# Kernel tuning notes

Hardware: AMD Instinct MI355X
Metric: run time of the kernel (lower is better)

The kernel has to match this reference:

```python
import jax, jax.numpy as jnp
import numpy as np

B, L, D, H, Dh = 4, 2048, 1024, 16, 64
DECAY_LR, A_LR, V_LR, G_LR = 64, 64, 32, 128
EPS_GN = 0.00064


def _lora(x, A, Bm, b, act):
    h = x @ A.T
    if act is not None:
        h = act(h)
    y = h @ Bm.T
    return y if b is None else y + b


def setup_inputs() -> dict:
    key = jax.random.key(0)
    ks = jax.random.split(key, 32)
    n = lambda k, shape, s=0.02: (jax.random.normal(k, shape, jnp.float32) * s)
    return {
        "x": n(ks[0], (B, L, D), 1.0),
        "v_first": n(ks[1], (B, L, H, Dh), 1.0),
        "x_r": n(ks[2], (1, 1, D)), "x_w": n(ks[3], (1, 1, D)),
        "x_k": n(ks[4], (1, 1, D)), "x_v": n(ks[5], (1, 1, D)),
        "x_a": n(ks[6], (1, 1, D)), "x_g": n(ks[7], (1, 1, D)),
        "k_k": n(ks[8], (H, Dh), 0.5), "k_a": n(ks[9], (H, Dh), 0.5),
        "r_k": n(ks[10], (H, Dh), 0.5),
        "Wr": n(ks[11], (D, D)), "Wk": n(ks[12], (D, D)),
        "Wv": n(ks[13], (D, D)), "Wo": n(ks[14], (D, D)),
        "gn_w": 1.0 + n(ks[15], (H, Dh)), "gn_b": n(ks[16], (H, Dh)),
        "w_A": n(ks[17], (DECAY_LR, D)), "w_B": n(ks[18], (D, DECAY_LR)), "w_b": n(ks[19], (D,)),
        "v_A": n(ks[20], (V_LR, D)), "v_B": n(ks[21], (D, V_LR)), "v_b": n(ks[22], (D,)),
        "a_A": n(ks[23], (A_LR, D)), "a_B": n(ks[24], (D, A_LR)), "a_b": n(ks[25], (D,)),
        "g_A": n(ks[26], (G_LR, D)), "g_B": n(ks[27], (D, G_LR)),
    }


def reference(x, v_first, x_r, x_w, x_k, x_v, x_a, x_g, k_k, k_a, r_k,
              Wr, Wk, Wv, Wo, gn_w, gn_b,
              w_A, w_B, w_b, v_A, v_B, v_b, a_A, a_B, a_b, g_A, g_B):
    Bx, Lx, Dx = x.shape
    # token shift (no cache -> zero-padded shift)
    x_prev = jnp.concatenate([jnp.zeros_like(x[:, :1]), x[:, :-1]], axis=1)
    xx = x_prev - x
    xr = x + xx * x_r
    xw = x + xx * x_w
    xk = x + xx * x_k
    xv = x + xx * x_v
    xa = x + xx * x_a
    xg = x + xx * x_g

    r = (xr @ Wr.T).reshape(Bx, Lx, H, Dh)
    k = (xk @ Wk.T).reshape(Bx, Lx, H, Dh)
    v = (xv @ Wv.T).reshape(Bx, Lx, H, Dh)
    iclr = jax.nn.sigmoid(_lora(xa, a_A, a_B, a_b, None)).reshape(Bx, Lx, H, Dh)
    gate = _lora(xg, g_A, g_B, None, jax.nn.sigmoid)  # (B,L,D)

    # layer_idx > 0: residual value mixing with v_first
    vv = jax.nn.sigmoid(_lora(xv, v_A, v_B, v_b, None)).reshape(Bx, Lx, H, Dh)
    v = v + (v_first - v) * vv

    w = jnp.exp(-0.606531 * jax.nn.sigmoid(
        _lora(xw, w_A, w_B, w_b, jnp.tanh)).reshape(Bx, Lx, H, Dh))

    kkn = k * k_k
    kk = kkn / jnp.maximum(jnp.linalg.norm(kkn, axis=-1, keepdims=True), 1e-7)
    k = k * (1.0 + (iclr - 1.0) * k_a)
    a = -kk
    b = kk * iclr

    # WKV7 generalized delta-rule scan over time
    def step(state, inp):
        rt, wt, kt, vt, at, bt = inp  # each (B,H,Dh)
        sa = jnp.einsum('bhij,bhj->bhi', state, at)
        state = (state * wt[:, :, None, :]
                 + vt[..., :, None] * kt[..., None, :]
                 + sa[..., :, None] * bt[..., None, :])
        y = jnp.einsum('bhij,bhj->bhi', state, rt)
        return state, y

    tr = lambda z: jnp.swapaxes(z, 0, 1)  # (B,L,H,Dh) -> (L,B,H,Dh)
    state0 = jnp.zeros((Bx, H, Dh, Dh), x.dtype)
    _, ys = jax.lax.scan(step, state0, (tr(r), tr(w), tr(k), tr(v), tr(a), tr(b)))
    out = jnp.swapaxes(ys, 0, 1)  # (B,L,H,Dh)

    # per-head layernorm (group norm), eps = 0.00064
    mean = out.mean(axis=-1, keepdims=True)
    var = out.var(axis=-1, keepdims=True)
    out = gn_w * (out - mean) / jnp.sqrt(var + EPS_GN) + gn_b

    out = out + jnp.sum(r * k * r_k, axis=-1, keepdims=True) * v
    out = out.reshape(Bx, Lx, Dx)
    return (out * gate) @ Wo.T
```

## Files before the change

kernel.cpp:

```cpp
#include <hip/hip_runtime.h>
#include <cmath>


#define DEV __device__ __forceinline__

typedef unsigned short u16;
typedef unsigned int u32;
typedef __bf16 bf16x8 __attribute__((ext_vector_type(8)));
typedef float f32x4 __attribute__((ext_vector_type(4)));

constexpr int Bx = 4, Lx = 2048, Dx = 1024, Hx = 16, Dh = 64;
constexpr int NTOK = Bx * Lx;
constexpr float EPS_GN = 0.00064f;
constexpr int STEP_U16 = 384;
constexpr int TB = 16;
constexpr int NB = Lx / TB;
constexpr int BATCH_U16 = TB * STEP_U16;

DEV float bf2f(u16 u) { union { u32 i; float f; } c; c.i = ((u32)u) << 16; return c.f; }
DEV u16 f2bf(float f) {
    union { float f; u32 i; } c; c.f = f;
    u32 r = c.i + 0x7FFFu + ((c.i >> 16) & 1u);
    return (u16)(r >> 16);
}
DEV void unpack2(u32 u, float& a, float& b) {
    union { u32 i; float f; } c0, c1;
    c0.i = u << 16; c1.i = u & 0xFFFF0000u;
    a = c0.f; b = c1.f;
}

template <int CTRL>
DEV float dpp_add(float v) {
    int p = __builtin_amdgcn_update_dpp(0, __float_as_int(v), CTRL, 0xF, 0xF, true);
    return v + __int_as_float(p);
}

DEV float xor32_add(float x) {
    float a = x, b = x;
    asm volatile("s_nop 1\n\tv_permlane32_swap_b32 %0, %1" : "+v"(a), "+v"(b));
    return a + b;
}

DEV float red32(float x) {
    x = dpp_add<0xB1>(x);
    x = dpp_add<0x4E>(x);
    x = dpp_add<0x141>(x);
    x = dpp_add<0x140>(x);
    return xor32_add(x);
}

__global__ __launch_bounds__(256) void conv_kernel(
    const float* s0, const float* s1, const float* s2, const float* s3,
    const float* s4, const float* s5, const float* s6, const float* s7,
    const float* s8, const float* s9, const float* s10, const float* s11,
    u16* d0, u16* d1, u16* d2, u16* d3, u16* d4, u16* d5, u16* d6, u16* d7,
    u16* d8, u16* d9, u16* d10, u16* d11)
{
    const float* srcs[12] = {s0,s1,s2,s3,s4,s5,s6,s7,s8,s9,s10,s11};
    u16* dsts[12] = {d0,d1,d2,d3,d4,d5,d6,d7,d8,d9,d10,d11};
    const int ns[12] = {65536,65536,32768,32768,65536,65536,131072,131072,
                        1048576,1048576,1048576,1048576};
    int t = blockIdx.y;
    int i = (blockIdx.x * 256 + threadIdx.x) * 4;
    if (i >= ns[t]) return;
    float4 v = *(const float4*)(srcs[t] + i);
    ushort4 o;
    o.x = f2bf(v.x); o.y = f2bf(v.y); o.z = f2bf(v.z); o.w = f2bf(v.w);
    *(ushort4*)(dsts[t] + i) = o;
}

__global__ __launch_bounds__(256) void mix_kernel(
    const float* __restrict__ x,
    const float* __restrict__ mr, const float* __restrict__ mw, const float* __restrict__ mk,
    const float* __restrict__ mv, const float* __restrict__ ma, const float* __restrict__ mg,
    u16* __restrict__ XR, u16* __restrict__ XW, u16* __restrict__ XK,
    u16* __restrict__ XV, u16* __restrict__ XA, u16* __restrict__ XG)
{
    int gi = blockIdx.x * 256 + threadIdx.x;
    int n  = gi >> 8;
    int d4 = (gi & 255) << 2;
    int l  = n & (Lx - 1);
    size_t o = (size_t)n * Dx + d4;
    float4 xc = *(const float4*)(x + o);
    float4 xp = make_float4(0.f, 0.f, 0.f, 0.f);
    if (l != 0) xp = *(const float4*)(x + o - Dx);
    float dx0 = xp.x - xc.x, dx1 = xp.y - xc.y, dx2 = xp.z - xc.z, dx3 = xp.w - xc.w;
    const float* mvs[6] = {mr, mw, mk, mv, ma, mg};
    u16* dsts[6] = {XR, XW, XK, XV, XA, XG};
#pragma unroll
    for (int j = 0; j < 6; ++j) {
        float4 m = *(const float4*)(mvs[j] + d4);
        ushort4 r;
        r.x = f2bf(fmaf(dx0, m.x, xc.x));
        r.y = f2bf(fmaf(dx1, m.y, xc.y));
        r.z = f2bf(fmaf(dx2, m.z, xc.z));
        r.w = f2bf(fmaf(dx3, m.w, xc.w));
        *(ushort4*)(dsts[j] + o) = r;
    }
}

template <int BN, int ACT, bool BIAS, bool F32OUT>
DEV void gemm_body(const u16* __restrict__ A, const u16* __restrict__ B16,
                   const float* __restrict__ bias, void* __restrict__ Cv,
                   int M, int N, int K, int bx, int by)
{
    constexpr int BM = 128, BK = 32;
    constexpr int WGM = (BN == 128) ? 2 : 4;
    constexpr int WGN = (BN == 128) ? 2 : 1;
    constexpr int WTM = BM / WGM, WTN = BN / WGN;
    constexpr int ITM = WTM / 16, ITN = WTN / 16;
    __shared__ __align__(16) u16 Asm[BM * BK];
    __shared__ __align__(16) u16 Bsm[BN * BK];
    const int tid = threadIdx.x;
    const int wid = tid >> 6, lane = tid & 63;
    const int q = lane >> 4, r16 = lane & 15;
    const size_t m0 = (size_t)bx * BM;
    const size_t n0 = (size_t)by * BN;
    const int wm = (wid % WGM) * WTM;
    const int wn = (wid / WGM) * WTN;
    f32x4 acc[ITM][ITN];
    const f32x4 zf = {0.f, 0.f, 0.f, 0.f};
#pragma unroll
    for (int i = 0; i < ITM; ++i)
#pragma unroll
        for (int j = 0; j < ITN; ++j) acc[i][j] = zf;

    for (int k0 = 0; k0 < K; k0 += BK) {
#pragma unroll
        for (int it = 0; it < 2; ++it) {
            int base = it * 2048 + wid * 512;
            int pp = base + lane * 8;
            int row = pp >> 5, col = pp & 31;
            __builtin_amdgcn_global_load_lds(
                (const __attribute__((address_space(1))) void*)(A + (m0 + row) * K + k0 + col),
                (__attribute__((address_space(3))) void*)(Asm + base), 16, 0, 0);
        }
#pragma unroll
        for (int it = 0; it < (BN * BK + 2047) / 2048; ++it) {
            int base = it * 2048 + wid * 512;
            if (BN * BK >= 2048 || base < BN * BK) {
                int pp = base + lane * 8;
                int row = pp >> 5, col = pp & 31;
                __builtin_amdgcn_global_load_lds(
                    (const __attribute__((address_space(1))) void*)(B16 + (n0 + row) * K + k0 + col),
                    (__attribute__((address_space(3))) void*)(Bsm + base), 16, 0, 0);
            }
        }
        __syncthreads();
        bf16x8 af[ITM], bfr[ITN];
#pragma unroll
        for (int im = 0; im < ITM; ++im)
            af[im] = *(const bf16x8*)&Asm[(wm + im * 16 + r16) * BK + q * 8];
#pragma unroll
        for (int in = 0; in < ITN; ++in)
            bfr[in] = *(const bf16x8*)&Bsm[(wn + in * 16 + r16) * BK + q * 8];
#pragma unroll
        for (int im = 0; im < ITM; ++im)
#pragma unroll
            for (int in = 0; in < ITN; ++in)
                acc[im][in] = __builtin_amdgcn_mfma_f32_16x16x32_bf16(af[im], bfr[in], acc[im][in], 0, 0, 0);
        __syncthreads();
    }
#pragma unroll
    for (int im = 0; im < ITM; ++im) {
#pragma unroll
        for (int in = 0; in < ITN; ++in) {
#pragma unroll
            for (int e = 0; e < 4; ++e) {
                size_t row = m0 + wm + im * 16 + q * 4 + e;
                size_t col = n0 + wn + in * 16 + r16;
                float val = acc[im][in][e];
                if constexpr (BIAS) val += bias[col];
                if constexpr (ACT == 1) val = 1.f / (1.f + __expf(-val));
                else if constexpr (ACT == 2) val = tanhf(val);
                else if constexpr (ACT == 3) val = __expf(-0.606531f / (1.f + __expf(-val)));
                if constexpr (F32OUT) ((float*)Cv)[row * (size_t)N + col] = val;
                else ((u16*)Cv)[row * (size_t)N + col] = f2bf(val);
            }
        }
    }
}

DEV void gemm_body_rt(const u16* __restrict__ A, const u16* __restrict__ B16,
                      const float* __restrict__ bias, u16* __restrict__ C,
                      int N, int K, int act, int bx, int by)
{
    constexpr int BM = 128, BN = 128, BK = 32;
    constexpr int ITM = 4, ITN = 4;
    __shared__ __align__(16) u16 Asm[BM * BK];
    __shared__ __align__(16) u16 Bsm[BN * BK];
    const int tid = threadIdx.x;
    const int wid = tid >> 6, lane = tid & 63;
    const int q = lane >> 4, r16 = lane & 15;
    const size_t m0 = (size_t)bx * BM;
    const size_t n0 = (size_t)by * BN;
    const int wm = (wid % 2) * 64;
    const int wn = (wid / 2) * 64;
    f32x4 acc[ITM][ITN];
    const f32x4 zf = {0.f, 0.f, 0.f, 0.f};
#pragma unroll
    for (int i = 0; i < ITM; ++i)
#pragma unroll
        for (int j = 0; j < ITN; ++j) acc[i][j] = zf;

    for (int k0 = 0; k0 < K; k0 += BK) {
#pragma unroll
        for (int it = 0; it < 2; ++it) {
            int base = it * 2048 + wid * 512;
            int pp = base + lane * 8;
            int row = pp >> 5, col = pp & 31;
            __builtin_amdgcn_global_load_lds(
                (const __attribute__((address_space(1))) void*)(A + (m0 + row) * K + k0 + col),
                (__attribute__((address_space(3))) void*)(Asm + base), 16, 0, 0);
        }
#pragma unroll
        for (int it = 0; it < 2; ++it) {
            int base = it * 2048 + wid * 512;
            int pp = base + lane * 8;
            int row = pp >> 5, col = pp & 31;
            __builtin_amdgcn_global_load_lds(
                (const __attribute__((address_space(1))) void*)(B16 + (n0 + row) * K + k0 + col),
                (__attribute__((address_space(3))) void*)(Bsm + base), 16, 0, 0);
        }
        __syncthreads();
        bf16x8 af[ITM], bfr[ITN];
#pragma unroll
        for (int im = 0; im < ITM; ++im)
            af[im] = *(const bf16x8*)&Asm[(wm + im * 16 + r16) * BK + q * 8];
#pragma unroll
        for (int in = 0; in < ITN; ++in)
            bfr[in] = *(const bf16x8*)&Bsm[(wn + in * 16 + r16) * BK + q * 8];
#pragma unroll
        for (int im = 0; im < ITM; ++im)
#pragma unroll
            for (int in = 0; in < ITN; ++in)
                acc[im][in] = __builtin_amdgcn_mfma_f32_16x16x32_bf16(af[im], bfr[in], acc[im][in], 0, 0, 0);
        __syncthreads();
    }
#pragma unroll
    for (int im = 0; im < ITM; ++im) {
#pragma unroll
        for (int in = 0; in < ITN; ++in) {
#pragma unroll
            for (int e = 0; e < 4; ++e) {
                size_t row = m0 + wm + im * 16 + q * 4 + e;
                size_t col = n0 + wn + in * 16 + r16;
                float val = acc[im][in][e];
                if (bias) val += bias[col];
                if (act == 1) val = 1.f / (1.f + __expf(-val));
                else if (act == 3) val = __expf(-0.606531f / (1.f + __expf(-val)));
                C[row * (size_t)N + col] = f2bf(val);
            }
        }
    }
}

DEV void lora1_body(int cfg,
    const u16* __restrict__ XW, const u16* __restrict__ XA,
    const u16* __restrict__ XV, const u16* __restrict__ XG,
    const u16* __restrict__ wAB, const u16* __restrict__ aAB,
    const u16* __restrict__ vAB, const u16* __restrict__ gAB,
    u16* __restrict__ HW, u16* __restrict__ HA,
    u16* __restrict__ HV, u16* __restrict__ HG, int bx)
{
    constexpr int BM = 128, BK = 32, K = 1024;
    constexpr int ITM = 2, ITN = 4;
    const u16* A; const u16* Bm; u16* C; int ldC, Nv, act;
    if (cfg == 0)      { A = XW; Bm = wAB;            C = HW;      ldC = 64;  Nv = 64; act = 2; }
    else if (cfg == 1) { A = XA; Bm = aAB;            C = HA;      ldC = 64;  Nv = 64; act = 0; }
    else if (cfg == 2) { A = XV; Bm = vAB;            C = HV;      ldC = 32;  Nv = 32; act = 0; }
    else if (cfg == 3) { A = XG; Bm = gAB;            C = HG;      ldC = 128; Nv = 64; act = 1; }
    else               { A = XG; Bm = gAB + 64 * K;   C = HG + 64; ldC = 128; Nv = 64; act = 1; }

    __shared__ __align__(16) u16 Asm1[BM * BK];
    __shared__ __align__(16) u16 Bsm1[64 * BK];
    const int tid = threadIdx.x;
    const int wid = tid >> 6, lane = tid & 63;
    const int q = lane >> 4, r16 = lane & 15;
    const size_t m0 = (size_t)bx * BM;
    const int wm = wid * 32;
    f32x4 acc[ITM][ITN];
    const f32x4 zf = {0.f, 0.f, 0.f, 0.f};
#pragma unroll
    for (int i = 0; i < ITM; ++i)
#pragma unroll
        for (int j = 0; j < ITN; ++j) acc[i][j] = zf;

    for (int k0 = 0; k0 < K; k0 += BK) {
#pragma unroll
        for (int it = 0; it < 2; ++it) {
            int base = it * 2048 + wid * 512;
            int pp = base + lane * 8;
            int row = pp >> 5, col = pp & 31;
            __builtin_amdgcn_global_load_lds(
                (const __attribute__((address_space(1))) void*)(A + (m0 + row) * K + k0 + col),
                (__attribute__((address_space(3))) void*)(Asm1 + base), 16, 0, 0);
        }
        {
            int base = wid * 512;
            int pp = base + lane * 8;
            int row = pp >> 5, col = pp & 31;
            __builtin_amdgcn_global_load_lds(
                (const __attribute__((address_space(1))) void*)(Bm + row * K + k0 + col),
                (__attribute__((address_space(3))) void*)(Bsm1 + base), 16, 0, 0);
        }
        __syncthreads();
        bf16x8 af[ITM], bfr[ITN];
#pragma unroll
        for (int im = 0; im < ITM; ++im)
            af[im] = *(const bf16x8*)&Asm1[(wm + im * 16 + r16) * BK + q * 8];
#pragma unroll
        for (int in = 0; in < ITN; ++in)
            bfr[in] = *(const bf16x8*)&Bsm1[(in * 16 + r16) * BK + q * 8];
#pragma unroll
        for (int im = 0; im < ITM; ++im)
#pragma unroll
            for (int in = 0; in < ITN; ++in)
                acc[im][in] = __builtin_amdgcn_mfma_f32_16x16x32_bf16(af[im], bfr[in], acc[im][in], 0, 0, 0);
        __syncthreads();
    }
#pragma unroll
    for (int im = 0; im < ITM; ++im) {
#pragma unroll
        for (int in = 0; in < ITN; ++in) {
#pragma unroll
            for (int e = 0; e < 4; ++e) {
                size_t row = m0 + wm + im * 16 + q * 4 + e;
                int col = in * 16 + r16;
                if (col < Nv) {
                    float val = acc[im][in][e];
                    if (act == 1) val = 1.f / (1.f + __expf(-val));
                    else if (act == 2) val = tanhf(val);
                    C[row * (size_t)ldC + col] = f2bf(val);
                }
            }
        }
    }
}

__global__ __launch_bounds__(256) void proj_kernel(
    const u16* __restrict__ XR, const u16* __restrict__ XK, const u16* __restrict__ XV,
    const u16* __restrict__ XW, const u16* __restrict__ XA, const u16* __restrict__ XG,
    const u16* __restrict__ Wr16, const u16* __restrict__ Wk16, const u16* __restrict__ Wv16,
    const u16* __restrict__ wAB, const u16* __restrict__ aAB,
    const u16* __restrict__ vAB, const u16* __restrict__ gAB,
    u16* __restrict__ Rbuf, u16* __restrict__ Kbuf, u16* __restrict__ Vbuf,
    u16* __restrict__ HW, u16* __restrict__ HA, u16* __restrict__ HV, u16* __restrict__ HG)
{
    const int z = blockIdx.z;
    if (z < 3) {
        const u16* A; const u16* Bm; u16* C;
        if (z == 0)      { A = XR; Bm = Wr16; C = Rbuf; }
        else if (z == 1) { A = XK; Bm = Wk16; C = Kbuf; }
        else             { A = XV; Bm = Wv16; C = Vbuf; }
        gemm_body<128, 0, false, false>(A, Bm, nullptr, C, NTOK, 1024, 1024,
                                        blockIdx.x, blockIdx.y);
    } else {
        if (blockIdx.y >= 5) return;
        lora1_body(blockIdx.y, XW, XA, XV, XG, wAB, aAB, vAB, gAB, HW, HA, HV, HG,
                   blockIdx.x);
    }
}

__global__ __launch_bounds__(256) void lora2_kernel(
    const u16* __restrict__ HW, const u16* __restrict__ HA,
    const u16* __restrict__ HV, const u16* __restrict__ HG,
    const u16* __restrict__ wBB, const u16* __restrict__ aBB,
    const u16* __restrict__ vBB, const u16* __restrict__ gBB,
    const float* __restrict__ wb, const float* __restrict__ ab, const float* __restrict__ vb,
    u16* __restrict__ Wdec16, u16* __restrict__ ICLR,
    u16* __restrict__ VVb, u16* __restrict__ GATE)
{
    const int z = blockIdx.z;
    const u16* A; const u16* Bm; const float* bias; u16* C; int K, act;
    if (z == 0)      { A = HW; Bm = wBB; bias = wb;      C = Wdec16; K = 64;  act = 3; }
    else if (z == 1) { A = HA; Bm = aBB; bias = ab;      C = ICLR;   K = 64;  act = 1; }
    else if (z == 2) { A = HV; Bm = vBB; bias = vb;      C = VVb;    K = 32;  act = 1; }
    else             { A = HG; Bm = gBB; bias = nullptr; C = GATE;   K = 128; act = 0; }
    gemm_body_rt(A, Bm, bias, C, 1024, K, act, blockIdx.x, blockIdx.y);
}

__global__ __launch_bounds__(256) void gemm_out_kernel(
    const u16* __restrict__ A, const u16* __restrict__ B16, float* __restrict__ C)
{
    gemm_body<128, 0, false, true>(A, B16, nullptr, C, NTOK, 1024, 1024,
                                   blockIdx.x, blockIdx.y);
}

__global__ __launch_bounds__(256) void prep_pack_kernel(
    const u16* __restrict__ Kb, const u16* __restrict__ Vb,
    const u16* __restrict__ Rb, const u16* __restrict__ Wd16,
    const u16* __restrict__ ICLR, const u16* __restrict__ VVb, const float* __restrict__ vfirst,
    const float* __restrict__ k_k, const float* __restrict__ k_a,
    u16* __restrict__ stream)
{
    int g = blockIdx.x * 4 + (threadIdx.x >> 6);
    int lane = threadIdx.x & 63;
    int h = g & (Hx - 1);
    int n = g >> 4;
    size_t idx = (size_t)g * 64 + lane;
    int hd = h * 64 + lane;
    int l = n & (Lx - 1), b = n >> 11;
    size_t so = ((size_t)((b * 16 + h) * Lx + l)) * STEP_U16;

    float k = bf2f(Kb[idx]);
    float iclr = bf2f(ICLR[idx]);
    float kkn = k * k_k[hd];
    float s = kkn * kkn;
#pragma unroll
    for (int off = 32; off > 0; off >>= 1) s += __shfl_xor(s, off, 64);
    float nrm = fmaxf(sqrtf(s), 1e-7f);
    float kk = kkn / nrm;
    u16 knew = f2bf(k * (1.f + (iclr - 1.f) * k_a[hd]));
    float v = bf2f(Vb[idx]), vv = bf2f(VVb[idx]), vf = vfirst[idx];
    u16 vnew = f2bf(fmaf(vf - v, vv, v));
    stream[so + lane]       = Rb[idx];
    stream[so + 64 + lane]  = knew;
    stream[so + 128 + lane] = f2bf(-kk);
    stream[so + 192 + lane] = f2bf(kk * iclr);
    stream[so + 256 + lane] = vnew;
    stream[so + 320 + lane] = Wd16[idx];
}

__global__ __launch_bounds__(256, 2) void scan_kernel(
    const u16* __restrict__ stream, float* __restrict__ Y)
{
    const int bid = blockIdx.x;
    const int xcd = bid & 7, slot = bid >> 3;
    const int bh = xcd + ((slot & 7) << 3);
    const int part = slot >> 3;
    const int tid = threadIdx.x;
    const int lane = tid & 63;
    const int w = tid >> 6;
    const int c = (lane & 15) | ((lane >> 1) & 16);
    const int rhalf = (lane >> 4) & 1;
    const int lr = w * 2 + rhalf;
    const int row = part * 8 + lr;
    const size_t sbase = (size_t)bh * Lx * STEP_U16;
    const size_t ybase = (size_t)(bh >> 4) * ((size_t)Lx * Dx) + (size_t)(bh & 15) * 64;

    __shared__ __align__(16) u16 sbuf[2 * BATCH_U16];
    __shared__ __align__(16) float yp[TB * 8 * 36];

    float S0 = 0.f, S1 = 0.f;

    {
        const u16* g = stream + sbase;
#pragma unroll
        for (int cc = 0; cc < 3; ++cc) {
            const u16* gp = g + (3 * w + cc) * 512 + lane * 8;
            u16* lp = sbuf + (3 * w + cc) * 512;
            __builtin_amdgcn_global_load_lds(
                (const __attribute__((address_space(1))) void*)gp,
                (__attribute__((address_space(3))) void*)lp, 16, 0, 0);
        }
    }

    for (int bt = 0; bt < NB; ++bt) {
        const int cur = bt & 1;
        __syncthreads();
        if (bt + 1 < NB) {
            const u16* g = stream + sbase + (size_t)(bt + 1) * BATCH_U16;
            u16* lbase = sbuf + (1 - cur) * BATCH_U16;
#pragma unroll
            for (int cc = 0; cc < 3; ++cc) {
                const u16* gp = g + (3 * w + cc) * 512 + lane * 8;
                u16* lp = lbase + (3 * w + cc) * 512;
                __builtin_amdgcn_global_load_lds(
                    (const __attribute__((address_space(1))) void*)gp,
                    (__attribute__((address_space(3))) void*)lp, 16, 0, 0);
            }
        }
        const u16* bp = sbuf + cur * BATCH_U16;
        const u16* cp = bp + c * 2;
        u32 r2 = *(const u32*)(cp);
        u32 k2 = *(const u32*)(cp + 64);
        u32 a2 = *(const u32*)(cp + 128);
        u32 b2 = *(const u32*)(cp + 192);
        u32 w2 = *(const u32*)(cp + 320);
        float v = bf2f(bp[256 + row]);
#pragma unroll
        for (int s = 0; s < TB; ++s) {
            u32 nr = 0, nk = 0, na = 0, nb = 0, nw = 0;
            float nv = 0.f;
            if (s + 1 < TB) {
                const u16* np = cp + (s + 1) * STEP_U16;
                nr = *(const u32*)(np);
                nk = *(const u32*)(np + 64);
                na = *(const u32*)(np + 128);
                nb = *(const u32*)(np + 192);
                nw = *(const u32*)(np + 320);
                nv = bf2f(bp[(s + 1) * STEP_U16 + 256 + row]);
            }
            float rr0, rr1, kk0, kk1, aa0, aa1, bb0, bb1, ww0, ww1;
            unpack2(r2, rr0, rr1);
            unpack2(k2, kk0, kk1);
            unpack2(a2, aa0, aa1);
            unpack2(b2, bb0, bb1);
            unpack2(w2, ww0, ww1);
            float sa = fmaf(S1, aa1, S0 * aa0);
            sa = red32(sa);
            float t0 = fmaf(v, kk0, sa * bb0);
            float t1 = fmaf(v, kk1, sa * bb1);
            S0 = fmaf(S0, ww0, t0);
            S1 = fmaf(S1, ww1, t1);
            float y = fmaf(S1, rr1, S0 * rr0);
            yp[(s * 8 + lr) * 36 + c] = y;
            r2 = nr; k2 = nk; a2 = na; b2 = nb; w2 = nw; v = nv;
        }
        __syncthreads();
        if (tid < TB * 8) {
            const float* rp = &yp[tid * 36];
            f32x4 a4 = *(const f32x4*)(rp);
#pragma unroll
            for (int i = 1; i < 8; ++i) {
                f32x4 t4 = *(const f32x4*)(rp + i * 4);
                a4 += t4;
            }
            float yy = (a4[0] + a4[1]) + (a4[2] + a4[3]);
            int s = tid >> 3, j = tid & 7;
            Y[ybase + (size_t)(bt * TB + s) * Dx + part * 8 + j] = yy;
        }
    }
}

__global__ __launch_bounds__(256) void gnorm_kernel(
    const float* __restrict__ Y, const u16* __restrict__ Rb,
    const u16* __restrict__ stream, const float* __restrict__ r_k,
    const float* __restrict__ gnw, const float* __restrict__ gnb,
    u16* __restrict__ GATE_OG)
{
    int g = blockIdx.x * 4 + (threadIdx.x >> 6);
    int lane = threadIdx.x & 63;
    int h = g & (Hx - 1);
    int n = g >> 4;
    size_t idx = (size_t)g * 64 + lane;
    int hd = h * 64 + lane;
    int l = n & (Lx - 1), b = n >> 11;
    size_t so = ((size_t)((b * 16 + h) * Lx + l)) * STEP_U16;
    float y = Y[idx];
    float r = bf2f(Rb[idx]);
    float k = bf2f(stream[so + 64 + lane]);
    float v = bf2f(stream[so + 256 + lane]);
    float rkr = r * k * r_k[hd];
    float s1 = y, s2 = y * y, s3 = rkr;
#pragma unroll
    for (int off = 32; off > 0; off >>= 1) {
        s1 += __shfl_xor(s1, off, 64);
        s2 += __shfl_xor(s2, off, 64);
        s3 += __shfl_xor(s3, off, 64);
    }
    float mean = s1 * (1.f / 64.f);
    float var  = s2 * (1.f / 64.f) - mean * mean;
    float inv = 1.f / sqrtf(var + EPS_GN);
    float o = gnw[hd] * ((y - mean) * inv) + gnb[hd];
    o += s3 * v;
    GATE_OG[idx] = f2bf(o * bf2f(GATE_OG[idx]));
}

extern "C" void kernel_launch(void* const* d_in, const int* in_sizes, int n_in,
                              void* d_out, int out_size, void* d_ws, size_t ws_size,
                              hipStream_t stream_)
{
    const float* x      = (const float*)d_in[0];
    const float* vfirst = (const float*)d_in[1];
    const float* x_r = (const float*)d_in[2];
    const float* x_w = (const float*)d_in[3];
    const float* x_k = (const float*)d_in[4];
    const float* x_v = (const float*)d_in[5];
    const float* x_a = (const float*)d_in[6];
    const float* x_g = (const float*)d_in[7];
    const float* k_k = (const float*)d_in[8];
    const float* k_a = (const float*)d_in[9];
    const float* r_k = (const float*)d_in[10];
    const float* Wr  = (const float*)d_in[11];
    const float* Wk  = (const float*)d_in[12];
    const float* Wv  = (const float*)d_in[13];
    const float* Wo  = (const float*)d_in[14];
    const float* gnw = (const float*)d_in[15];
    const float* gnb = (const float*)d_in[16];
    const float* wA  = (const float*)d_in[17];
    const float* wB  = (const float*)d_in[18];
    const float* wb  = (const float*)d_in[19];
    const float* vA  = (const float*)d_in[20];
    const float* vB  = (const float*)d_in[21];
    const float* vb  = (const float*)d_in[22];
    const float* aA  = (const float*)d_in[23];
    const float* aB  = (const float*)d_in[24];
    const float* ab  = (const float*)d_in[25];
    const float* gA  = (const float*)d_in[26];
    const float* gB  = (const float*)d_in[27];

    char* ws = (char*)d_ws;
    const size_t SLOT = (size_t)NTOK * Dx * 2;
    u16* XR = (u16*)(ws + 0 * SLOT);
    u16* XW = (u16*)(ws + 1 * SLOT);
    u16* XK = (u16*)(ws + 2 * SLOT);
    u16* XV = (u16*)(ws + 3 * SLOT);
    u16* XA = (u16*)(ws + 4 * SLOT);
    u16* XG = (u16*)(ws + 5 * SLOT);
    u16* STREAM = (u16*)(ws + 0 * SLOT);
    u16* Rbuf = (u16*)(ws + 6 * SLOT);
    u16* Kbuf = (u16*)(ws + 7 * SLOT);
    u16* Vbuf = (u16*)(ws + 8 * SLOT);
    u16* HW = (u16*)(ws + 9 * SLOT);
    u16* HA = HW + (size_t)NTOK * 64;
    u16* HV = HA + (size_t)NTOK * 64;
    u16* HG = HV + (size_t)NTOK * 32;
    u16* Wo16 = HG + (size_t)NTOK * 128;
    u16* SW = (u16*)(ws + 9 * SLOT + 8 * 1024 * 1024);
    u16* wAB = SW;
    u16* wBB = wAB + 65536;
    u16* vAB = wBB + 65536;
    u16* vBB = vAB + 32768;
    u16* aAB = vBB + 32768;
    u16* aBB = aAB + 65536;
    u16* gAB = aBB + 65536;
    u16* gBB = gAB + 131072;
    u16* Wr16 = (u16*)(ws + 9 * SLOT + 10 * 1024 * 1024);
    u16* Wk16 = Wr16 + 1048576;
    u16* Wv16 = Wk16 + 1048576;
    u16* Wdec16 = (u16*)(ws + 10 * SLOT);
    u16* ICLR   = (u16*)(ws + 11 * SLOT);
    u16* VVb    = (u16*)(ws + 12 * SLOT);
    float* Yb   = (float*)(ws + 10 * SLOT);
    u16* GATE   = (u16*)(ws + 13 * SLOT);

    dim3 blk(256);
    conv_kernel<<<dim3(1024, 12), blk, 0, stream_>>>(
        wA, wB, vA, vB, aA, aB, gA, gB, Wr, Wk, Wv, Wo,
        wAB, wBB, vAB, vBB, aAB, aBB, gAB, gBB, Wr16, Wk16, Wv16, Wo16);
    mix_kernel<<<(NTOK * Dx / 4) / 256, blk, 0, stream_>>>(x, x_r, x_w, x_k, x_v, x_a, x_g,
                                                           XR, XW, XK, XV, XA, XG);
    proj_kernel<<<dim3(64, 8, 4), blk, 0, stream_>>>(
        XR, XK, XV, XW, XA, XG, Wr16, Wk16, Wv16, wAB, aAB, vAB, gAB,
        Rbuf, Kbuf, Vbuf, HW, HA, HV, HG);
    lora2_kernel<<<dim3(64, 8, 4), blk, 0, stream_>>>(
        HW, HA, HV, HG, wBB, aBB, vBB, gBB, wb, ab, vb, Wdec16, ICLR, VVb, GATE);

    prep_pack_kernel<<<(NTOK * Hx) / 4, blk, 0, stream_>>>(Kbuf, Vbuf, Rbuf, Wdec16, ICLR, VVb,
                                                           vfirst, k_k, k_a, STREAM);
    scan_kernel<<<512, blk, 0, stream_>>>(STREAM, Yb);
    gnorm_kernel<<<(NTOK * Hx) / 4, blk, 0, stream_>>>(Yb, Rbuf, STREAM, r_k, gnw, gnb, GATE);
    gemm_out_kernel<<<dim3(64, 8), blk, 0, stream_>>>(GATE, Wo16, (float*)d_out);
}
```

Measured before the change: 700.7 us.

## Double-buffer LDS in GEMM bodies and fuse weight conversion with token mix

All GEMM bodies (projection, lora, output) now use two LDS buffers carved from a shared pool. The next K tile is prefetched via global_load_lds while MFMAs run on the current tile, which removes one barrier per K step. The separate weight-conversion and token-mix kernels are merged into one launch keyed on block index. The pool raises LDS use per block, which may reduce occupancy, and the overlap depends on the async LDS loads being correctly waited on at the barrier.

Result: no change. 691.3 us (-1.3%).

```diff
diff --git a/kernel.cpp b/kernel.cpp
--- a/kernel.cpp
+++ b/kernel.cpp
@@ -49,58 +49,61 @@
     return xor32_add(x);
 }
 
-__global__ __launch_bounds__(256) void conv_kernel(
+__global__ __launch_bounds__(256) void convmix_kernel(
+    const float* __restrict__ x,
+    const float* __restrict__ mr, const float* __restrict__ mw, const float* __restrict__ mk,
+    const float* __restrict__ mv, const float* __restrict__ ma, const float* __restrict__ mg,
+    u16* __restrict__ XR, u16* __restrict__ XW, u16* __restrict__ XK,
+    u16* __restrict__ XV, u16* __restrict__ XA, u16* __restrict__ XG,
     const float* s0, const float* s1, const float* s2, const float* s3,
     const float* s4, const float* s5, const float* s6, const float* s7,
     const float* s8, const float* s9, const float* s10, const float* s11,
     u16* d0, u16* d1, u16* d2, u16* d3, u16* d4, u16* d5, u16* d6, u16* d7,
     u16* d8, u16* d9, u16* d10, u16* d11)
 {
-    const float* srcs[12] = {s0,s1,s2,s3,s4,s5,s6,s7,s8,s9,s10,s11};
-    u16* dsts[12] = {d0,d1,d2,d3,d4,d5,d6,d7,d8,d9,d10,d11};
-    const int ns[12] = {65536,65536,32768,32768,65536,65536,131072,131072,
-                        1048576,1048576,1048576,1048576};
-    int t = blockIdx.y;
-    int i = (blockIdx.x * 256 + threadIdx.x) * 4;
-    if (i >= ns[t]) return;
-    float4 v = *(const float4*)(srcs[t] + i);
-    ushort4 o;
-    o.x = f2bf(v.x); o.y = f2bf(v.y); o.z = f2bf(v.z); o.w = f2bf(v.w);
-    *(ushort4*)(dsts[t] + i) = o;
-}
-
-__global__ __launch_bounds__(256) void mix_kernel(
-    const float* __restrict__ x,
-    const float* __restrict__ mr, const float* __restrict__ mw, const float* __restrict__ mk,
-    const float* __restrict__ mv, const float* __restrict__ ma, const float* __restrict__ mg,
-    u16* __restrict__ XR, u16* __restrict__ XW, u16* __restrict__ XK,
-    u16* __restrict__ XV, u16* __restrict__ XA, u16* __restrict__ XG)
-{
-    int gi = blockIdx.x * 256 + threadIdx.x;
-    int n  = gi >> 8;
-    int d4 = (gi & 255) << 2;
-    int l  = n & (Lx - 1);
-    size_t o = (size_t)n * Dx + d4;
-    float4 xc = *(const float4*)(x + o);
-    float4 xp = make_float4(0.f, 0.f, 0.f, 0.f);
-    if (l != 0) xp = *(const float4*)(x + o - Dx);
-    float dx0 = xp.x - xc.x, dx1 = xp.y - xc.y, dx2 = xp.z - xc.z, dx3 = xp.w - xc.w;
-    const float* mvs[6] = {mr, mw, mk, mv, ma, mg};
-    u16* dsts[6] = {XR, XW, XK, XV, XA, XG};
-#pragma unroll
-    for (int j = 0; j < 6; ++j) {
-        float4 m = *(const float4*)(mvs[j] + d4);
-        ushort4 r;
-        r.x = f2bf(fmaf(dx0, m.x, xc.x));
-        r.y = f2bf(fmaf(dx1, m.y, xc.y));
-        r.z = f2bf(fmaf(dx2, m.z, xc.z));
-        r.w = f2bf(fmaf(dx3, m.w, xc.w));
-        *(ushort4*)(dsts[j] + o) = r;
+    const int bid = blockIdx.x;
+    const int tid = threadIdx.x;
+    if (bid < 8192) {
+        int gi = bid * 256 + tid;
+        int n  = gi >> 8;
+        int d4v = (gi & 255) << 2;
+        int l  = n & (Lx - 1);
+        size_t o = (size_t)n * Dx + d4v;
+        float4 xc = *(const float4*)(x + o);
+        float4 xp = make_float4(0.f, 0.f, 0.f, 0.f);
+        if (l != 0) xp = *(const float4*)(x + o - Dx);
+        float dx0 = xp.x - xc.x, dx1 = xp.y - xc.y, dx2 = xp.z - xc.z, dx3 = xp.w - xc.w;
+        const float* mvs[6] = {mr, mw, mk, mv, ma, mg};
+        u16* dsts[6] = {XR, XW, XK, XV, XA, XG};
+#pragma unroll
+        for (int j = 0; j < 6; ++j) {
+            float4 m = *(const float4*)(mvs[j] + d4v);
+            ushort4 r;
+            r.x = f2bf(fmaf(dx0, m.x, xc.x));
+            r.y = f2bf(fmaf(dx1, m.y, xc.y));
+            r.z = f2bf(fmaf(dx2, m.z, xc.z));
+            r.w = f2bf(fmaf(dx3, m.w, xc.w));
+            *(ushort4*)(dsts[j] + o) = r;
+        }
+    } else {
+        const float* srcs[12] = {s0,s1,s2,s3,s4,s5,s6,s7,s8,s9,s10,s11};
+        u16* dsts[12] = {d0,d1,d2,d3,d4,d5,d6,d7,d8,d9,d10,d11};
+        const int ns[12] = {65536,65536,32768,32768,65536,65536,131072,131072,
+                            1048576,1048576,1048576,1048576};
+        int cb = bid - 8192;
+        int t = cb >> 10;
+        int i = ((cb & 1023) * 256 + tid) * 4;
+        if (i >= ns[t]) return;
+        float4 v = *(const float4*)(srcs[t] + i);
+        ushort4 o;
+        o.x = f2bf(v.x); o.y = f2bf(v.y); o.z = f2bf(v.z); o.w = f2bf(v.w);
+        *(ushort4*)(dsts[t] + i) = o;
     }
 }
 
 template <int BN, int ACT, bool BIAS, bool F32OUT>
-DEV void gemm_body(const u16* __restrict__ A, const u16* __restrict__ B16,
+DEV void gemm_body(u16* __restrict__ smem,
+                   const u16* __restrict__ A, const u16* __restrict__ B16,
                    const float* __restrict__ bias, void* __restrict__ Cv,
                    int M, int N, int K, int bx, int by)
 {
@@ -109,8 +112,8 @@
     constexpr int WGN = (BN == 128) ? 2 : 1;
     constexpr int WTM = BM / WGM, WTN = BN / WGN;
     constexpr int ITM = WTM / 16, ITN = WTN / 16;
-    __shared__ __align__(16) u16 Asm[BM * BK];
-    __shared__ __align__(16) u16 Bsm[BN * BK];
+    u16* Asm0 = smem;
+    u16* Bsm0 = smem + 2 * BM * BK;
     const int tid = threadIdx.x;
     const int wid = tid >> 6, lane = tid & 63;
     const int q = lane >> 4, r16 = lane & 15;
@@ -125,41 +128,70 @@
 #pragma unroll
         for (int j = 0; j < ITN; ++j) acc[i][j] = zf;
 
-    for (int k0 = 0; k0 < K; k0 += BK) {
-#pragma unroll
-        for (int it = 0; it < 2; ++it) {
-            int base = it * 2048 + wid * 512;
+#pragma unroll
+    for (int it = 0; it < 2; ++it) {
+        int base = it * 2048 + wid * 512;
+        int pp = base + lane * 8;
+        int row = pp >> 5, col = pp & 31;
+        __builtin_amdgcn_global_load_lds(
+            (const __attribute__((address_space(1))) void*)(A + (m0 + row) * K + col),
+            (__attribute__((address_space(3))) void*)(Asm0 + base), 16, 0, 0);
+    }
+#pragma unroll
+    for (int it = 0; it < (BN * BK + 2047) / 2048; ++it) {
+        int base = it * 2048 + wid * 512;
+        if (BN * BK >= 2048 || base < BN * BK) {
             int pp = base + lane * 8;
             int row = pp >> 5, col = pp & 31;
             __builtin_amdgcn_global_load_lds(
-                (const __attribute__((address_space(1))) void*)(A + (m0 + row) * K + k0 + col),
-                (__attribute__((address_space(3))) void*)(Asm + base), 16, 0, 0);
-        }
-#pragma unroll
-        for (int it = 0; it < (BN * BK + 2047) / 2048; ++it) {
-            int base = it * 2048 + wid * 512;
-            if (BN * BK >= 2048 || base < BN * BK) {
+                (const __attribute__((address_space(1))) void*)(B16 + (n0 + row) * K + col),
+                (__attribute__((address_space(3))) void*)(Bsm0 + base), 16, 0, 0);
+        }
+    }
+
+    int t = 0;
+    for (int k0 = 0; k0 < K; k0 += BK, ++t) {
+        const int cur = t & 1;
+        __syncthreads();
+        if (k0 + BK < K) {
+            u16* An = Asm0 + (cur ^ 1) * (BM * BK);
+            u16* Bn = Bsm0 + (cur ^ 1) * (BN * BK);
+            const int kn = k0 + BK;
+#pragma unroll
+            for (int it = 0; it < 2; ++it) {
+                int base = it * 2048 + wid * 512;
                 int pp = base + lane * 8;
                 int row = pp >> 5, col = pp & 31;
                 __builtin_amdgcn_global_load_lds(
-                    (const __attribute__((address_space(1))) void*)(B16 + (n0 + row) * K + k0 + col),
-                    (__attribute__((address_space(3))) void*)(Bsm + base), 16, 0, 0);
-            }
-        }
-        __syncthreads();
+                    (const __attribute__((address_space(1))) void*)(A + (m0 + row) * K + kn + col),
+                    (__attribute__((address_space(3))) void*)(An + base), 16, 0, 0);
+            }
+#pragma unroll
+            for (int it = 0; it < (BN * BK + 2047) / 2048; ++it) {
+                int base = it * 2048 + wid * 512;
+                if (BN * BK >= 2048 || base < BN * BK) {
+                    int pp = base + lane * 8;
+                    int row = pp >> 5, col = pp & 31;
+                    __builtin_amdgcn_global_load_lds(
+                        (const __attribute__((address_space(1))) void*)(B16 + (n0 + row) * K + kn + col),
+                        (__attribute__((address_space(3))) void*)(Bn + base), 16, 0, 0);
+                }
+            }
+        }
+        const u16* Ac = Asm0 + cur * (BM * BK);
+        const u16* Bc = Bsm0 + cur * (BN * BK);
         bf16x8 af[ITM], bfr[ITN];
 #pragma unroll
         for (int im = 0; im < ITM; ++im)
-            af[im] = *(const bf16x8*)&Asm[(wm + im * 16 + r16) * BK + q * 8];
+            af[im] = *(const bf16x8*)&Ac[(wm + im * 16 + r16) * BK + q * 8];
 #pragma unroll
         for (int in = 0; in < ITN; ++in)
-            bfr[in] = *(const bf16x8*)&Bsm[(wn + in * 16 + r16) * BK + q * 8];
+            bfr[in] = *(const bf16x8*)&Bc[(wn + in * 16 + r16) * BK + q * 8];
 #pragma unroll
         for (int im = 0; im < ITM; ++im)
 #pragma unroll
             for (int in = 0; in < ITN; ++in)
                 acc[im][in] = __builtin_amdgcn_mfma_f32_16x16x32_bf16(af[im], bfr[in], acc[im][in], 0, 0, 0);
-        __syncthreads();
     }
 #pragma unroll
     for (int im = 0; im < ITM; ++im) {
@@ -181,19 +213,20 @@
     }
 }
 
-DEV void gemm_body_rt(const u16* __restrict__ A, const u16* __restrict__ B16,
+DEV void gemm_body_rt(u16* __restrict__ smem,
+                      const u16* __restrict__ A, const u16* __restrict__ B16,
                       const float* __restrict__ bias, u16* __restrict__ C,
                       int N, int K, int act, int bx, int by)
 {
-    constexpr int BM = 128, BN = 128, BK = 32;
+    constexpr int BM = 128, BK = 32;
     constexpr int ITM = 4, ITN = 4;
-    __shared__ __align__(16) u16 Asm[BM * BK];
-    __shared__ __align__(16) u16 Bsm[BN * BK];
+    u16* Asm0 = smem;
+    u16* Bsm0 = smem + 2 * BM * BK;
     const int tid = threadIdx.x;
     const int wid = tid >> 6, lane = tid & 63;
     const int q = lane >> 4, r16 = lane & 15;
     const size_t m0 = (size_t)bx * BM;
-    const size_t n0 = (size_t)by * BN;
+    const size_t n0 = (size_t)by * 128;
     const int wm = (wid % 2) * 64;
     const int wn = (wid / 2) * 64;
     f32x4 acc[ITM][ITN];
@@ -203,39 +236,54 @@
 #pragma unroll
         for (int j = 0; j < ITN; ++j) acc[i][j] = zf;
 
-    for (int k0 = 0; k0 < K; k0 += BK) {
-#pragma unroll
-        for (int it = 0; it < 2; ++it) {
-            int base = it * 2048 + wid * 512;
-            int pp = base + lane * 8;
-            int row = pp >> 5, col = pp & 31;
-            __builtin_amdgcn_global_load_lds(
-                (const __attribute__((address_space(1))) void*)(A + (m0 + row) * K + k0 + col),
-                (__attribute__((address_space(3))) void*)(Asm + base), 16, 0, 0);
-        }
-#pragma unroll
-        for (int it = 0; it < 2; ++it) {
-            int base = it * 2048 + wid * 512;
-            int pp = base + lane * 8;
-            int row = pp >> 5, col = pp & 31;
-            __builtin_amdgcn_global_load_lds(
-                (const __attribute__((address_space(1))) void*)(B16 + (n0 + row) * K + k0 + col),
-                (__attribute__((address_space(3))) void*)(Bsm + base), 16, 0, 0);
-        }
+#pragma unroll
+    for (int it = 0; it < 2; ++it) {
+        int base = it * 2048 + wid * 512;
+        int pp = base + lane * 8;
+        int row = pp >> 5, col = pp & 31;
+        __builtin_amdgcn_global_load_lds(
+            (const __attribute__((address_space(1))) void*)(A + (m0 + row) * K + col),
+            (__attribute__((address_space(3))) void*)(Asm0 + base), 16, 0, 0);
+        __builtin_amdgcn_global_load_lds(
+            (const __attribute__((address_space(1))) void*)(B16 + (n0 + row) * K + col),
+            (__attribute__((address_space(3))) void*)(Bsm0 + base), 16, 0, 0);
+    }
+
+    int t = 0;
+    for (int k0 = 0; k0 < K; k0 += BK, ++t) {
+        const int cur = t & 1;
         __syncthreads();
+        if (k0 + BK < K) {
+            u16* An = Asm0 + (cur ^ 1) * (BM * BK);
+            u16* Bn = Bsm0 + (cur ^ 1) * (BM * BK);
+            const int kn = k0 + BK;
+#pragma unroll
+            for (int it = 0; it < 2; ++it) {
+                int base = it * 2048 + wid * 512;
+                int pp = base + lane * 8;
+                int row = pp >> 5, col = pp & 31;
+                __builtin_amdgcn_global_load_lds(
+                    (const __attribute__((address_space(1))) void*)(A + (m0 + row) * K + kn + col),
+                    (__attribute__((address_space(3))) void*)(An + base), 16, 0, 0);
+                __builtin_amdgcn_global_load_lds(
+                    (const __attribute__((address_space(1))) void*)(B16 + (n0 + row) * K + kn + col),
+                    (__attribute__((address_space(3))) void*)(Bn + base), 16, 0, 0);
+            }
+        }
+        const u16* Ac = Asm0 + cur * (BM * BK);
+        const u16* Bc = Bsm0 + cur * (BM * BK);
         bf16x8 af[ITM], bfr[ITN];
 #pragma unroll
         for (int im = 0; im < ITM; ++im)
-            af[im] = *(const bf16x8*)&Asm[(wm + im * 16 + r16) * BK + q * 8];
+            af[im] = *(const bf16x8*)&Ac[(wm + im * 16 + r16) * BK + q * 8];
 #pragma unroll
         for (int in = 0; in < ITN; ++in)
-            bfr[in] = *(const bf16x8*)&Bsm[(wn + in * 16 + r16) * BK + q * 8];
+            bfr[in] = *(const bf16x8*)&Bc[(wn + in * 16 + r16) * BK + q * 8];
 #pragma unroll
         for (int im = 0; im < ITM; ++im)
 #pragma unroll
             for (int in = 0; in < ITN; ++in)
                 acc[im][in] = __builtin_amdgcn_mfma_f32_16x16x32_bf16(af[im], bfr[in], acc[im][in], 0, 0, 0);
-        __syncthreads();
     }
 #pragma unroll
     for (int im = 0; im < ITM; ++im) {
@@ -255,7 +303,7 @@
     }
 }
 
-DEV void lora1_body(int cfg,
+DEV void lora1_body(u16* __restrict__ smem, int cfg,
     const u16* __restrict__ XW, const u16* __restrict__ XA,
     const u16* __restrict__ XV, const u16* __restrict__ XG,
     const u16* __restrict__ wAB, const u16* __restrict__ aAB,
@@ -272,8 +320,8 @@
     else if (cfg == 3) { A = XG; Bm = gAB;            C = HG;      ldC = 128; Nv = 64; act = 1; }
     else               { A = XG; Bm = gAB + 64 * K;   C = HG + 64; ldC = 128; Nv = 64; act = 1; }
 
-    __shared__ __align__(16) u16 Asm1[BM * BK];
-    __shared__ __align__(16) u16 Bsm1[64 * BK];
+    u16* Asm0 = smem;
+    u16* Bsm0 = smem + 2 * BM * BK;
     const int tid = threadIdx.x;
     const int wid = tid >> 6, lane = tid & 63;
     const int q = lane >> 4, r16 = lane & 15;
@@ -286,38 +334,64 @@
 #pragma unroll
         for (int j = 0; j < ITN; ++j) acc[i][j] = zf;
 
-    for (int k0 = 0; k0 < K; k0 += BK) {
-#pragma unroll
-        for (int it = 0; it < 2; ++it) {
-            int base = it * 2048 + wid * 512;
-            int pp = base + lane * 8;
-            int row = pp >> 5, col = pp & 31;
-            __builtin_amdgcn_global_load_lds(
-                (const __attribute__((address_space(1))) void*)(A + (m0 + row) * K + k0 + col),
-                (__attribute__((address_space(3))) void*)(Asm1 + base), 16, 0, 0);
-        }
-        {
-            int base = wid * 512;
-            int pp = base + lane * 8;
-            int row = pp >> 5, col = pp & 31;
-            __builtin_amdgcn_global_load_lds(
-                (const __attribute__((address_space(1))) void*)(Bm + row * K + k0 + col),
-                (__attribute__((address_space(3))) void*)(Bsm1 + base), 16, 0, 0);
-        }
+#pragma unroll
+    for (int it = 0; it < 2; ++it) {
+        int base = it * 2048 + wid * 512;
+        int pp = base + lane * 8;
+        int row = pp >> 5, col = pp & 31;
+        __builtin_amdgcn_global_load_lds(
+            (const __attribute__((address_space(1))) void*)(A + (m0 + row) * K + col),
+            (__attribute__((address_space(3))) void*)(Asm0 + base), 16, 0, 0);
+    }
+    {
+        int base = wid * 512;
+        int pp = base + lane * 8;
+        int row = pp >> 5, col = pp & 31;
+        __builtin_amdgcn_global_load_lds(
+            (const __attribute__((address_space(1))) void*)(Bm + row * K + col),
+            (__attribute__((address_space(3))) void*)(Bsm0 + base), 16, 0, 0);
+    }
+
+    int t = 0;
+    for (int k0 = 0; k0 < K; k0 += BK, ++t) {
+        const int cur = t & 1;
         __syncthreads();
+        if (k0 + BK < K) {
+            u16* An = Asm0 + (cur ^ 1) * (BM * BK);
+            u16* Bn = Bsm0 + (cur ^ 1) * 2048;
+            const int kn = k0 + BK;
+#pragma unroll
+            for (int it = 0; it < 2; ++it) {
+                int base = it * 2048 + wid * 512;
+                int pp = base + lane * 8;
+                int row = pp >> 5, col = pp & 31;
+                __builtin_amdgcn_global_load_lds(
+                    (const __attribute__((address_space(1))) void*)(A + (m0 + row) * K + kn + col),
+                    (__attribute__((address_space(3))) void*)(An + base), 16, 0, 0);
+            }
+            {
+                int base = wid * 512;
+                int pp = base + lane * 8;
+                int row = pp >> 5, col = pp & 31;
+                __builtin_amdgcn_global_load_lds(
+                    (const __attribute__((address_space(1))) void*)(Bm + row * K + kn + col),
+                    (__attribute__((address_space(3))) void*)(Bn + base), 16, 0, 0);
+            }
+        }
+        const u16* Ac = Asm0 + cur * (BM * BK);
+        const u16* Bc = Bsm0 + cur * 2048;
         bf16x8 af[ITM], bfr[ITN];
 #pragma unroll
         for (int im = 0; im < ITM; ++im)
-            af[im] = *(const bf16x8*)&Asm1[(wm + im * 16 + r16) * BK + q * 8];
+            af[im] = *(const bf16x8*)&Ac[(wm + im * 16 + r16) * BK + q * 8];
 #pragma unroll
         for (int in = 0; in < ITN; ++in)
-            bfr[in] = *(const bf16x8*)&Bsm1[(in * 16 + r16) * BK + q * 8];
+            bfr[in] = *(const bf16x8*)&Bc[(in * 16 + r16) * BK + q * 8];
 #pragma unroll
         for (int im = 0; im < ITM; ++im)
 #pragma unroll
             for (int in = 0; in < ITN; ++in)
                 acc[im][in] = __builtin_amdgcn_mfma_f32_16x16x32_bf16(af[im], bfr[in], acc[im][in], 0, 0, 0);
-        __syncthreads();
     }
 #pragma unroll
     for (int im = 0; im < ITM; ++im) {
@@ -347,17 +421,18 @@
     u16* __restrict__ Rbuf, u16* __restrict__ Kbuf, u16* __restrict__ Vbuf,
     u16* __restrict__ HW, u16* __restrict__ HA, u16* __restrict__ HV, u16* __restrict__ HG)
 {
+    __shared__ __align__(16) u16 pool[16384];
     const int z = blockIdx.z;
     if (z < 3) {
         const u16* A; const u16* Bm; u16* C;
         if (z == 0)      { A = XR; Bm = Wr16; C = Rbuf; }
         else if (z == 1) { A = XK; Bm = Wk16; C = Kbuf; }
         else             { A = XV; Bm = Wv16; C = Vbuf; }
-        gemm_body<128, 0, false, false>(A, Bm, nullptr, C, NTOK, 1024, 1024,
+        gemm_body<128, 0, false, false>(pool, A, Bm, nullptr, C, NTOK, 1024, 1024,
                                         blockIdx.x, blockIdx.y);
     } else {
         if (blockIdx.y >= 5) return;
-        lora1_body(blockIdx.y, XW, XA, XV, XG, wAB, aAB, vAB, gAB, HW, HA, HV, HG,
+        lora1_body(pool, blockIdx.y, XW, XA, XV, XG, wAB, aAB, vAB, gAB, HW, HA, HV, HG,
                    blockIdx.x);
     }
 }
@@ -371,19 +446,21 @@
     u16* __restrict__ Wdec16, u16* __restrict__ ICLR,
     u16* __restrict__ VVb, u16* __restrict__ GATE)
 {
+    __shared__ __align__(16) u16 pool[16384];
     const int z = blockIdx.z;
     const u16* A; const u16* Bm; const float* bias; u16* C; int K, act;
     if (z == 0)      { A = HW; Bm = wBB; bias = wb;      C = Wdec16; K = 64;  act = 3; }
     else if (z == 1) { A = HA; Bm = aBB; bias = ab;      C = ICLR;   K = 64;  act = 1; }
     else if (z == 2) { A = HV; Bm = vBB; bias = vb;      C = VVb;    K = 32;  act = 1; }
     else             { A = HG; Bm = gBB; bias = nullptr; C = GATE;   K = 128; act = 0; }
-    gemm_body_rt(A, Bm, bias, C, 1024, K, act, blockIdx.x, blockIdx.y);
+    gemm_body_rt(pool, A, Bm, bias, C, 1024, K, act, blockIdx.x, blockIdx.y);
 }
 
 __global__ __launch_bounds__(256) void gemm_out_kernel(
     const u16* __restrict__ A, const u16* __restrict__ B16, float* __restrict__ C)
 {
-    gemm_body<128, 0, false, true>(A, B16, nullptr, C, NTOK, 1024, 1024,
+    __shared__ __align__(16) u16 pool[16384];
+    gemm_body<128, 0, false, true>(pool, A, B16, nullptr, C, NTOK, 1024, 1024,
                                    blockIdx.x, blockIdx.y);
 }
 
@@ -627,11 +704,10 @@
     u16* GATE   = (u16*)(ws + 13 * SLOT);
 
     dim3 blk(256);
-    conv_kernel<<<dim3(1024, 12), blk, 0, stream_>>>(
+    convmix_kernel<<<dim3(20480), blk, 0, stream_>>>(
+        x, x_r, x_w, x_k, x_v, x_a, x_g, XR, XW, XK, XV, XA, XG,
         wA, wB, vA, vB, aA, aB, gA, gB, Wr, Wk, Wv, Wo,
         wAB, wBB, vAB, vBB, aAB, aBB, gAB, gBB, Wr16, Wk16, Wv16, Wo16);
-    mix_kernel<<<(NTOK * Dx / 4) / 256, blk, 0, stream_>>>(x, x_r, x_w, x_k, x_v, x_a, x_g,
-                                                           XR, XW, XK, XV, XA, XG);
     proj_kernel<<<dim3(64, 8, 4), blk, 0, stream_>>>(
         XR, XK, XV, XW, XA, XG, Wr16, Wk16, Wv16, wAB, aAB, vAB, gAB,
         Rbuf, Kbuf, Vbuf, HW, HA, HV, HG);
```
